# Performance work log

Measured on AMD Instinct MI355X. Metric: run time of the kernel, lower is better.

Reference implementation:

```python
import jax, jax.numpy as jnp
import numpy as np

N = 50000      # nodes
E = 800000     # random edges (self-loops appended inside reference)
DIN = 128
DH = 32        # per-head hidden dim of layer 1
H = 8          # heads
DOUT = 32      # output dim (layer 2, concat=False)
NEG_SLOPE = 0.2


def segment_softmax(e, seg, num):
    # numerically stable softmax over variable-size segments (per-destination)
    m = jax.ops.segment_max(e, seg, num_segments=num)
    m = jnp.where(jnp.isfinite(m), m, jnp.zeros_like(m))
    ex = jnp.exp(e - m[seg])
    s = jax.ops.segment_sum(ex, seg, num_segments=num)
    return ex / (s[seg] + 1e-16)


def gatv2_conv(x, src, dst, Wl, Wr, att, bias, heads, dim, concat):
    n = x.shape[0]
    xl = (x @ Wl).reshape(n, heads, dim)   # source transform
    xr = (x @ Wr).reshape(n, heads, dim)   # target transform
    z = xl[src] + xr[dst]                  # [E, H, D] gather per edge
    z = jnp.where(z > 0, z, NEG_SLOPE * z) # LeakyReLU BEFORE attention vector (GATv2)
    e = jnp.einsum('ehd,hd->eh', z, att)   # attention logits [E, H]
    alpha = segment_softmax(e, dst, n)     # softmax over in-edges of each dst
    out = jax.ops.segment_sum(alpha[:, :, None] * xl[src], dst, num_segments=n)
    if concat:
        return out.reshape(n, heads * dim) + bias
    return out.mean(axis=1) + bias


def setup_inputs() -> dict:
    key = jax.random.key(0)
    ks = jax.random.split(key, 12)
    x = jax.random.normal(ks[0], (N, DIN), dtype=jnp.float32)
    edge_index = jax.random.randint(ks[1], (2, E), 0, N, dtype=jnp.int64)
    s = 0.05
    Wl1 = jax.random.normal(ks[2], (DIN, H * DH), dtype=jnp.float32) * s
    Wr1 = jax.random.normal(ks[3], (DIN, H * DH), dtype=jnp.float32) * s
    att1 = jax.random.normal(ks[4], (H, DH), dtype=jnp.float32) * s
    b1 = jnp.zeros((H * DH,), dtype=jnp.float32)
    Wl2 = jax.random.normal(ks[5], (H * DH, H * DOUT), dtype=jnp.float32) * s
    Wr2 = jax.random.normal(ks[6], (H * DH, H * DOUT), dtype=jnp.float32) * s
    att2 = jax.random.normal(ks[7], (H, DOUT), dtype=jnp.float32) * s
    b2 = jnp.zeros((DOUT,), dtype=jnp.float32)
    return {"x": x, "edge_index": edge_index, "Wl1": Wl1, "Wr1": Wr1,
            "att1": att1, "b1": b1, "Wl2": Wl2, "Wr2": Wr2,
            "att2": att2, "b2": b2}


def reference(x, edge_index, Wl1, Wr1, att1, b1, Wl2, Wr2, att2, b2):
    n = x.shape[0]
    loops = jnp.arange(n, dtype=edge_index.dtype)
    src = jnp.concatenate([edge_index[0], loops])  # PyG adds self-loops by default
    dst = jnp.concatenate([edge_index[1], loops])
    h = gatv2_conv(x, src, dst, Wl1, Wr1, att1, b1, H, DH, concat=True)
    h = jax.nn.elu(h)
    out = gatv2_conv(h, src, dst, Wl2, Wr2, att2, b2, H, DOUT, concat=False)
    return out
```

## Files before the change

kernel.cpp:

```cpp
#include <hip/hip_runtime.h>
#include <hip/hip_bf16.h>

typedef __hip_bfloat16 bf16;
typedef __attribute__((ext_vector_type(8))) short bf16x8;
typedef __attribute__((ext_vector_type(4))) float f32x4;
typedef __attribute__((ext_vector_type(2))) float f32x2;

#define N_NODES 50000
#define E_RAW   800000
#define E_TOT   850000
#define H_HEADS 8
#define F_DIM   256
#define NB_SCAN 196

__device__ __forceinline__ float loadF(const void* p, size_t i, int f32) {
    return f32 ? ((const float*)p)[i] : __bfloat162float(((const bf16*)p)[i]);
}
__device__ __forceinline__ int loadI(const void* p, size_t i, int is32) {
    return is32 ? ((const int*)p)[i] : (int)((const long long*)p)[i];
}
__device__ __forceinline__ float uasf(unsigned u) { return __uint_as_float(u); }
__device__ __forceinline__ unsigned f2bfbits(float f) {
    unsigned u = __float_as_uint(f);
    return (u + 0x7fff + ((u >> 16) & 1)) >> 16;
}
__device__ __forceinline__ short f2bfs(float f) {
    unsigned u = __float_as_uint(f);
    return (short)((u + 0x7fff + ((u >> 16) & 1)) >> 16);
}

__global__ void detect_zero(const void* __restrict__ x, const void* __restrict__ ei,
                            int* __restrict__ flags, int* __restrict__ counts) {
    int gid = blockIdx.x * 256 + threadIdx.x;
    if (gid < N_NODES) counts[gid] = 0;
    if (blockIdx.x != 0) return;
    __shared__ int sf[2];
    int t = threadIdx.x;
    if (t < 2) sf[t] = 0;
    __syncthreads();
    const unsigned short* xs = (const unsigned short*)x;
    int f32 = 0;
    for (int i = t; i < 8192; i += 256) {
        unsigned e = (xs[i] >> 7) & 0xFF;
        if (e >= 134) f32 = 1;
    }
    const int* eii = (const int*)ei;
    int odd = 0;
    for (int i = t; i < 1024; i += 256)
        if (eii[2 * i + 1] != 0) odd = 1;
    if (f32) atomicOr(&sf[0], 1);
    if (odd) atomicOr(&sf[1], 1);
    __syncthreads();
    if (t < 2) flags[t] = sf[t];
}

__global__ void xcvt(const void* __restrict__ x, bf16* __restrict__ xb,
                     const int* __restrict__ flags) {
    const int f32 = flags[0];
    int i = blockIdx.x * 256 + threadIdx.x;
    if (i >= (N_NODES * 128) / 8) return;
    unsigned short* dst = (unsigned short*)xb + (size_t)i * 8;
    if (f32) {
        const float* xp = (const float*)x + (size_t)i * 8;
        float4 v0 = *(const float4*)xp;
        float4 v1 = *(const float4*)(xp + 4);
        uint4 o;
        o.x = f2bfbits(v0.x) | (f2bfbits(v0.y) << 16);
        o.y = f2bfbits(v0.z) | (f2bfbits(v0.w) << 16);
        o.z = f2bfbits(v1.x) | (f2bfbits(v1.y) << 16);
        o.w = f2bfbits(v1.z) | (f2bfbits(v1.w) << 16);
        *(uint4*)dst = o;
    } else {
        uint4 v = *(const uint4*)((const unsigned short*)x + (size_t)i * 8);
        *(uint4*)dst = v;
    }
}

__global__ void prep(const void* __restrict__ wl1, const void* __restrict__ wr1,
                     const void* __restrict__ wl2, const void* __restrict__ wr2,
                     const void* __restrict__ ei,
                     bf16* __restrict__ wb, int* __restrict__ counts,
                     unsigned short* __restrict__ rank,
                     const int* __restrict__ flags) {
    const int f32 = flags[0], is32 = flags[1];
    int gid = blockIdx.x * 256 + threadIdx.x;
    if (gid < E_TOT) {
        int d = (gid < E_RAW) ? loadI(ei, (size_t)E_RAW + gid, is32) : (gid - E_RAW);
        rank[gid] = (unsigned short)atomicAdd(&counts[d], 1);
    }
    for (size_t j = gid; j < 196608; j += (size_t)gridDim.x * 256) {
        const void* src; size_t off, base;
        int k, n;
        if (j < 65536) {
            int half = j >= 32768;
            off = j - (size_t)half * 32768;
            src = half ? wr1 : wl1;
            k = (int)(off >> 8); n = half * 256 + (int)(off & 255);
            base = 0;
        } else {
            size_t jj = j - 65536;
            int half = jj >= 65536;
            off = jj - (size_t)half * 65536;
            src = half ? wr2 : wl2;
            k = (int)(off >> 8); n = half * 256 + (int)(off & 255);
            base = 65536;
        }
        int kb = k >> 5, jo = k & 7;
        int lane = ((k >> 3) & 3) * 16 + (n & 15);
        int ctg = n >> 4;
        size_t dst = base + (((size_t)(kb * 32 + ctg) * 64 + lane) * 8 + jo);
        wb[dst] = __float2bfloat16(loadF(src, off, f32));
    }
}

__global__ void scan1(const int* __restrict__ counts, int* __restrict__ rp,
                      int* __restrict__ bsum) {
    __shared__ int sm[256];
    int b = blockIdx.x, t = threadIdx.x;
    int i = b * 256 + t;
    int v = (i < N_NODES) ? counts[i] : 0;
    sm[t] = v; __syncthreads();
    for (int off = 1; off < 256; off <<= 1) {
        int u = (t >= off) ? sm[t - off] : 0;
        __syncthreads();
        sm[t] += u;
        __syncthreads();
    }
    int incl = sm[t];
    if (i < N_NODES) rp[i] = incl - v;
    if (t == 255) bsum[b] = incl;
}

__global__ void scan2(int* __restrict__ bsum) {
    __shared__ int sm[256];
    int t = threadIdx.x;
    int v = (t < NB_SCAN) ? bsum[t] : 0;
    sm[t] = v; __syncthreads();
    for (int off = 1; off < 256; off <<= 1) {
        int u = (t >= off) ? sm[t - off] : 0;
        __syncthreads();
        sm[t] += u;
        __syncthreads();
    }
    if (t < NB_SCAN) bsum[t] = sm[t] - v;
}

__global__ void scan3(int* __restrict__ rp, const int* __restrict__ bsum) {
    int b = blockIdx.x, t = threadIdx.x;
    int i = b * 256 + t;
    if (i < N_NODES) rp[i] += bsum[b];
    if (i == 0) rp[N_NODES] = E_TOT;
}

__global__ void fill(const void* __restrict__ ei, const int* __restrict__ rp,
                     const unsigned short* __restrict__ rank,
                     int* __restrict__ srcs, const int* __restrict__ flags) {
    const int is32 = flags[1];
    int e = blockIdx.x * 256 + threadIdx.x;
    if (e >= E_TOT + 64) return;
    if (e >= E_TOT) { srcs[e] = 0; return; }
    int s, d;
    if (e < E_RAW) { s = loadI(ei, e, is32); d = loadI(ei, (size_t)E_RAW + e, is32); }
    else           { s = d = e - E_RAW; }
    srcs[rp[d] + rank[e]] = s;
}

__launch_bounds__(256)
__global__ void gemm_mfma(const bf16* __restrict__ A, const bf16* __restrict__ Wsw,
                          bf16* __restrict__ Cl, bf16* __restrict__ Cr,
                          int M, int K) {
    const int tid = threadIdx.x;
    const int w = tid >> 6, lane = tid & 63, q = lane >> 4, l16 = lane & 15;
    const int bRow = blockIdx.x * 128 + (w >> 1) * 64;
    const int bCol = blockIdx.y * 128 + (w & 1) * 64;
    const int ctg0 = bCol >> 4;
    const short* Wp = (const short*)Wsw;
    const int nkb = K >> 5;
    int rows[4];
#pragma unroll
    for (int i = 0; i < 4; ++i) {
        int r = bRow + i * 16 + l16;
        rows[i] = r < M ? r : M - 1;
    }
    f32x4 acc[16] = {};
    for (int kb = 0; kb < nkb; ++kb) {
        bf16x8 a[4], b[4];
#pragma unroll
        for (int i = 0; i < 4; ++i)
            a[i] = *(const bf16x8*)((const short*)A + (size_t)rows[i] * K + q * 8 + kb * 32);
#pragma unroll
        for (int j = 0; j < 4; ++j)
            b[j] = *(const bf16x8*)(Wp + ((size_t)(kb * 32 + ctg0 + j) * 64 + lane) * 8);
#pragma unroll
        for (int i = 0; i < 4; ++i)
#pragma unroll
            for (int j = 0; j < 4; ++j)
                acc[i * 4 + j] =
                    __builtin_amdgcn_mfma_f32_16x16x32_bf16(b[j], a[i], acc[i * 4 + j], 0, 0, 0);
    }
    unsigned short* C = (unsigned short*)(bCol < 256 ? Cl : Cr);
    const int cBase = (bCol < 256 ? bCol : bCol - 256) + q * 4;
#pragma unroll
    for (int i = 0; i < 4; ++i) {
        int row = bRow + i * 16 + l16;
        if (row < M) {
#pragma unroll
            for (int j = 0; j < 4; ++j) {
                f32x4 v = acc[i * 4 + j];
                uint2 o;
                o.x = f2bfbits(v[0]) | (f2bfbits(v[1]) << 16);
                o.y = f2bfbits(v[2]) | (f2bfbits(v[3]) << 16);
                *(uint2*)(C + (size_t)row * 256 + cBase + j * 16) = o;
            }
        }
    }
}

#define EDGE(Q, PRED)                                                         \
    {                                                                         \
        f32x2 X0 = {uasf(Q.x << 16), uasf(Q.x & 0xffff0000u)};                \
        f32x2 X1 = {uasf(Q.y << 16), uasf(Q.y & 0xffff0000u)};                \
        f32x2 X2 = {uasf(Q.z << 16), uasf(Q.z & 0xffff0000u)};                \
        f32x2 X3 = {uasf(Q.w << 16), uasf(Q.w & 0xffff0000u)};                \
        f32x2 z0 = X0 + rv0, z1 = X1 + rv1, z2 = X2 + rv2, z3 = X3 + rv3;     \
        float qq = a0.x * fabsf(z0.x);                                        \
        qq = fmaf(a0.y, fabsf(z0.y), qq);                                     \
        qq = fmaf(a1.x, fabsf(z1.x), qq);                                     \
        qq = fmaf(a1.y, fabsf(z1.y), qq);                                     \
        qq = fmaf(a2.x, fabsf(z2.x), qq);                                     \
        qq = fmaf(a2.y, fabsf(z2.y), qq);                                     \
        qq = fmaf(a3.x, fabsf(z3.x), qq);                                     \
        qq = fmaf(a3.y, fabsf(z3.y), qq);                                     \
        f32x2 slv = a0 * X0;                                                  \
        slv += a1 * X1; slv += a2 * X2; slv += a3 * X3;                       \
        float pp = fmaf(0.6f, slv.x + slv.y, 0.4f * qq);                      \
        pp += __shfl_xor(pp, 1); pp += __shfl_xor(pp, 2);                     \
        float wv = (PRED) ? __expf(pp + cd) : 0.f;                            \
        den += wv;                                                            \
        f32x2 wv2 = {wv, wv};                                                 \
        n0 += wv2 * X0; n1 += wv2 * X1; n2 += wv2 * X2; n3 += wv2 * X3;       \
    }
__launch_bounds__(256)
__global__ void fused_attn(const int* __restrict__ rp, const int* __restrict__ srcs,
                           const bf16* __restrict__ xl, const bf16* __restrict__ xr,
                           const void* __restrict__ att, const void* __restrict__ bias,
                           void* __restrict__ outp, int mode,
                           const int* __restrict__ flags) {
    const int f32 = flags[0];
    const int tid = threadIdx.x, wid = tid >> 6, lane = tid & 63;
    const int sub = lane & 31;
    const int d = blockIdx.x * 8 + wid * 2 + (lane >> 5);

    const unsigned short* xru = (const unsigned short*)xr;
    uint4 xv = *(const uint4*)(xru + (size_t)d * 256 + sub * 8);
    f32x2 rv0 = {uasf(xv.x << 16), uasf(xv.x & 0xffff0000u)};
    f32x2 rv1 = {uasf(xv.y << 16), uasf(xv.y & 0xffff0000u)};
    f32x2 rv2 = {uasf(xv.z << 16), uasf(xv.z & 0xffff0000u)};
    f32x2 rv3 = {uasf(xv.w << 16), uasf(xv.w & 0xffff0000u)};
    f32x2 a0, a1, a2, a3;
    if (f32) {
        float4 t0 = *(const float4*)((const float*)att + sub * 8);
        float4 t1 = *(const float4*)((const float*)att + sub * 8 + 4);
        a0 = {t0.x, t0.y}; a1 = {t0.z, t0.w}; a2 = {t1.x, t1.y}; a3 = {t1.z, t1.w};
    } else {
        uint4 av = *(const uint4*)((const unsigned short*)att + sub * 8);
        a0 = {uasf(av.x << 16), uasf(av.x & 0xffff0000u)};
        a1 = {uasf(av.y << 16), uasf(av.y & 0xffff0000u)};
        a2 = {uasf(av.z << 16), uasf(av.z & 0xffff0000u)};
        a3 = {uasf(av.w << 16), uasf(av.w & 0xffff0000u)};
    }

    f32x2 tv = a0 * rv0;
    tv += a1 * rv1; tv += a2 * rv2; tv += a3 * rv3;
    float t = tv.x + tv.y;
    t += __shfl_xor(t, 1); t += __shfl_xor(t, 2);
    const float cd = 0.6f * t;

    const int start = rp[d], cnt = rp[d + 1] - start;
    int mA = __shfl(cnt, 0), mB = __shfl(cnt, 32);
    const int maxc = mA > mB ? mA : mB;
    const int* sp = srcs + start;
    const unsigned short* xlu = (const unsigned short*)xl + sub * 8;

    float den = 0.f;
    f32x2 n0 = {0,0}, n1 = {0,0}, n2 = {0,0}, n3 = {0,0};
    int i = 0;
    for (; i + 3 < maxc; i += 4) {
        int s0 = sp[i], s1 = sp[i + 1], s2 = sp[i + 2], s3 = sp[i + 3];
        uint4 q0 = *(const uint4*)(xlu + (size_t)s0 * 256);
        uint4 q1 = *(const uint4*)(xlu + (size_t)s1 * 256);
        uint4 q2 = *(const uint4*)(xlu + (size_t)s2 * 256);
        uint4 q3 = *(const uint4*)(xlu + (size_t)s3 * 256);
        EDGE(q0, i < cnt);
        EDGE(q1, i + 1 < cnt);
        EDGE(q2, i + 2 < cnt);
        EDGE(q3, i + 3 < cnt);
    }
    for (; i < maxc; ++i) {
        int s0 = sp[i];
        uint4 q0 = *(const uint4*)(xlu + (size_t)s0 * 256);
        EDGE(q0, i < cnt);
    }
    float rd = 1.f / (den + 1e-16f);
    float v[8] = {n0.x * rd, n0.y * rd, n1.x * rd, n1.y * rd,
                  n2.x * rd, n2.y * rd, n3.x * rd, n3.y * rd};

    if (mode == 1) {
        float b[8];
        if (f32) {
            float4 t0 = *(const float4*)((const float*)bias + sub * 8);
            float4 t1 = *(const float4*)((const float*)bias + sub * 8 + 4);
            b[0]=t0.x; b[1]=t0.y; b[2]=t0.z; b[3]=t0.w;
            b[4]=t1.x; b[5]=t1.y; b[6]=t1.z; b[7]=t1.w;
        } else {
            uint4 bv = *(const uint4*)((const unsigned short*)bias + sub * 8);
            b[0]=uasf(bv.x<<16); b[1]=uasf(bv.x&0xffff0000u);
            b[2]=uasf(bv.y<<16); b[3]=uasf(bv.y&0xffff0000u);
            b[4]=uasf(bv.z<<16); b[5]=uasf(bv.z&0xffff0000u);
            b[6]=uasf(bv.w<<16); b[7]=uasf(bv.w&0xffff0000u);
        }
        uint4 o;
        unsigned oo[4];
#pragma unroll
        for (int k = 0; k < 4; ++k) {
            float u0 = v[2*k]   + b[2*k];
            float u1 = v[2*k+1] + b[2*k+1];
            u0 = u0 > 0.f ? u0 : expm1f(u0);
            u1 = u1 > 0.f ? u1 : expm1f(u1);
            oo[k] = f2bfbits(u0) | (f2bfbits(u1) << 16);
        }
        o.x = oo[0]; o.y = oo[1]; o.z = oo[2]; o.w = oo[3];
        *(uint4*)((unsigned short*)outp + (size_t)d * 256 + sub * 8) = o;
    } else {
#pragma unroll
        for (int k = 0; k < 8; ++k) {
            v[k] += __shfl_xor(v[k], 4);
            v[k] += __shfl_xor(v[k], 8);
            v[k] += __shfl_xor(v[k], 16);
        }
        if (sub < 4) {
            int j = sub * 8;
            float o[8];
#pragma unroll
            for (int k = 0; k < 8; ++k)
                o[k] = v[k] * 0.125f + loadF(bias, j + k, f32);
            if (f32) {
                float4 o0 = {o[0], o[1], o[2], o[3]};
                float4 o1 = {o[4], o[5], o[6], o[7]};
                *(float4*)((float*)outp + (size_t)d * 32 + j)     = o0;
                *(float4*)((float*)outp + (size_t)d * 32 + j + 4) = o1;
            } else {
                uint4 ob;
                ob.x = f2bfbits(o[0]) | (f2bfbits(o[1]) << 16);
                ob.y = f2bfbits(o[2]) | (f2bfbits(o[3]) << 16);
                ob.z = f2bfbits(o[4]) | (f2bfbits(o[5]) << 16);
                ob.w = f2bfbits(o[6]) | (f2bfbits(o[7]) << 16);
                *(uint4*)((unsigned short*)outp + (size_t)d * 32 + j) = ob;
            }
        }
    }
}

extern "C" void kernel_launch(void* const* d_in, const int* in_sizes, int n_in,
                              void* d_out, int out_size, void* d_ws, size_t ws_size,
                              hipStream_t stream) {
    const void* x    = d_in[0];
    const void* ei   = d_in[1];
    const void* Wl1  = d_in[2];
    const void* Wr1  = d_in[3];
    const void* att1 = d_in[4];
    const void* b1   = d_in[5];
    const void* Wl2  = d_in[6];
    const void* Wr2  = d_in[7];
    const void* att2 = d_in[8];
    const void* b2   = d_in[9];

    char* p = (char*)d_ws;
    auto take = [&](size_t bytes) { char* r = p; p += (bytes + 255) & ~(size_t)255; return r; };
    int*  flags  = (int*) take(64 * sizeof(int));
    bf16* wb     = (bf16*)take(196608 * sizeof(bf16));
    bf16* xl     = (bf16*)take((size_t)N_NODES * F_DIM * sizeof(bf16));
    bf16* xr     = (bf16*)take((size_t)N_NODES * F_DIM * sizeof(bf16));
    bf16* h1     = (bf16*)take((size_t)N_NODES * F_DIM * sizeof(bf16));
    int*  rp     = (int*) take((N_NODES + 1) * sizeof(int));
    int*  counts = (int*) take(N_NODES * sizeof(int));
    int*  bsum   = (int*) take(256 * sizeof(int));
    unsigned short* rank = (unsigned short*)take((size_t)E_TOT * sizeof(unsigned short));
    int*  srcs   = (int*) take(((size_t)E_TOT + 64) * sizeof(int));

    bf16* W1sw = wb;
    bf16* W2sw = wb + 65536;
    bf16* xb   = h1;

    const int GB = (E_TOT + 255) / 256;

    detect_zero<<<196, 256, 0, stream>>>(x, ei, flags, counts);
    xcvt<<<(N_NODES * 128 / 8 + 255) / 256, 256, 0, stream>>>(x, xb, flags);
    prep<<<GB, 256, 0, stream>>>(Wl1, Wr1, Wl2, Wr2, ei, wb, counts, rank, flags);
    scan1<<<NB_SCAN, 256, 0, stream>>>(counts, rp, bsum);
    scan2<<<1, 256, 0, stream>>>(bsum);
    scan3<<<NB_SCAN, 256, 0, stream>>>(rp, bsum);
    fill<<<GB, 256, 0, stream>>>(ei, rp, rank, srcs, flags);

    dim3 ggrd((N_NODES + 127) / 128, 4);

    gemm_mfma<<<ggrd, 256, 0, stream>>>(xb, W1sw, xl, xr, N_NODES, 128);
    fused_attn<<<N_NODES / 8, 256, 0, stream>>>(rp, srcs, xl, xr, att1, b1, h1, 1, flags);

    gemm_mfma<<<ggrd, 256, 0, stream>>>(h1, W2sw, xl, xr, N_NODES, 256);
    fused_attn<<<N_NODES / 8, 256, 0, stream>>>(rp, srcs, xl, xr, att2, b2, d_out, 2, flags);
}
```

Baseline: 374.5 us.

## Process nodes in degree-sorted order with one node per wave, split edges across half-waves

Builds a degree histogram and counting-sorts nodes by descending in-degree, so the attention kernel visits heavy nodes first and keeps the waves in a block balanced. Each wave now handles a single destination node, with the two 32-lane halves taking alternate edges and combining their partial sums by shuffle. The old scheme ran two nodes per wave to the longer of the two lengths, which left lanes idle. The GEMM remaps its 1-D grid for XCD locality, and bf16 input x is read directly instead of being copied. Costs are extra scan work, an indirection through the order array, and atomics that make the node order nondeterministic.

Measured after the change: 535.7 us. +43.1%, slower.

```diff
diff --git a/kernel.cpp b/kernel.cpp
--- a/kernel.cpp
+++ b/kernel.cpp
@@ -24,15 +24,13 @@
     unsigned u = __float_as_uint(f);
     return (u + 0x7fff + ((u >> 16) & 1)) >> 16;
 }
-__device__ __forceinline__ short f2bfs(float f) {
-    unsigned u = __float_as_uint(f);
-    return (short)((u + 0x7fff + ((u >> 16) & 1)) >> 16);
-}
 
 __global__ void detect_zero(const void* __restrict__ x, const void* __restrict__ ei,
-                            int* __restrict__ flags, int* __restrict__ counts) {
+                            int* __restrict__ flags, int* __restrict__ counts,
+                            int* __restrict__ deghist) {
     int gid = blockIdx.x * 256 + threadIdx.x;
     if (gid < N_NODES) counts[gid] = 0;
+    if (gid < 256) deghist[gid] = 0;
     if (blockIdx.x != 0) return;
     __shared__ int sf[2];
     int t = threadIdx.x;
@@ -56,24 +54,19 @@
 
 __global__ void xcvt(const void* __restrict__ x, bf16* __restrict__ xb,
                      const int* __restrict__ flags) {
-    const int f32 = flags[0];
+    if (!flags[0]) return;
     int i = blockIdx.x * 256 + threadIdx.x;
     if (i >= (N_NODES * 128) / 8) return;
     unsigned short* dst = (unsigned short*)xb + (size_t)i * 8;
-    if (f32) {
-        const float* xp = (const float*)x + (size_t)i * 8;
-        float4 v0 = *(const float4*)xp;
-        float4 v1 = *(const float4*)(xp + 4);
-        uint4 o;
-        o.x = f2bfbits(v0.x) | (f2bfbits(v0.y) << 16);
-        o.y = f2bfbits(v0.z) | (f2bfbits(v0.w) << 16);
-        o.z = f2bfbits(v1.x) | (f2bfbits(v1.y) << 16);
-        o.w = f2bfbits(v1.z) | (f2bfbits(v1.w) << 16);
-        *(uint4*)dst = o;
-    } else {
-        uint4 v = *(const uint4*)((const unsigned short*)x + (size_t)i * 8);
-        *(uint4*)dst = v;
-    }
+    const float* xp = (const float*)x + (size_t)i * 8;
+    float4 v0 = *(const float4*)xp;
+    float4 v1 = *(const float4*)(xp + 4);
+    uint4 o;
+    o.x = f2bfbits(v0.x) | (f2bfbits(v0.y) << 16);
+    o.y = f2bfbits(v0.z) | (f2bfbits(v0.w) << 16);
+    o.z = f2bfbits(v1.x) | (f2bfbits(v1.y) << 16);
+    o.w = f2bfbits(v1.z) | (f2bfbits(v1.w) << 16);
+    *(uint4*)dst = o;
 }
 
 __global__ void prep(const void* __restrict__ wl1, const void* __restrict__ wr1,
@@ -114,12 +107,18 @@
 }
 
 __global__ void scan1(const int* __restrict__ counts, int* __restrict__ rp,
-                      int* __restrict__ bsum) {
+                      int* __restrict__ bsum, int* __restrict__ deghist) {
     __shared__ int sm[256];
+    __shared__ int lh[256];
     int b = blockIdx.x, t = threadIdx.x;
     int i = b * 256 + t;
     int v = (i < N_NODES) ? counts[i] : 0;
-    sm[t] = v; __syncthreads();
+    sm[t] = v; lh[t] = 0;
+    __syncthreads();
+    if (i < N_NODES) {
+        int dg = v < 255 ? v : 255;
+        atomicAdd(&lh[255 - dg], 1);
+    }
     for (int off = 1; off < 256; off <<= 1) {
         int u = (t >= off) ? sm[t - off] : 0;
         __syncthreads();
@@ -129,9 +128,10 @@
     int incl = sm[t];
     if (i < N_NODES) rp[i] = incl - v;
     if (t == 255) bsum[b] = incl;
-}
-
-__global__ void scan2(int* __restrict__ bsum) {
+    if (lh[t]) atomicAdd(&deghist[t], lh[t]);
+}
+
+__global__ void scan2(int* __restrict__ bsum, int* __restrict__ deghist) {
     __shared__ int sm[256];
     int t = threadIdx.x;
     int v = (t < NB_SCAN) ? bsum[t] : 0;
@@ -143,12 +143,29 @@
         __syncthreads();
     }
     if (t < NB_SCAN) bsum[t] = sm[t] - v;
-}
-
-__global__ void scan3(int* __restrict__ rp, const int* __restrict__ bsum) {
+    __syncthreads();
+    int hv = deghist[t];
+    sm[t] = hv; __syncthreads();
+    for (int off = 1; off < 256; off <<= 1) {
+        int u = (t >= off) ? sm[t - off] : 0;
+        __syncthreads();
+        sm[t] += u;
+        __syncthreads();
+    }
+    deghist[t] = sm[t] - hv;
+}
+
+__global__ void scan3(int* __restrict__ rp, const int* __restrict__ bsum,
+                      const int* __restrict__ counts, int* __restrict__ deghist,
+                      int* __restrict__ ord) {
     int b = blockIdx.x, t = threadIdx.x;
     int i = b * 256 + t;
-    if (i < N_NODES) rp[i] += bsum[b];
+    if (i < N_NODES) {
+        rp[i] += bsum[b];
+        int dg = counts[i]; dg = dg < 255 ? dg : 255;
+        int pos = atomicAdd(&deghist[255 - dg], 1);
+        ord[pos] = i;
+    }
     if (i == 0) rp[N_NODES] = E_TOT;
 }
 
@@ -157,8 +174,7 @@
                      int* __restrict__ srcs, const int* __restrict__ flags) {
     const int is32 = flags[1];
     int e = blockIdx.x * 256 + threadIdx.x;
-    if (e >= E_TOT + 64) return;
-    if (e >= E_TOT) { srcs[e] = 0; return; }
+    if (e >= E_TOT) return;
     int s, d;
     if (e < E_RAW) { s = loadI(ei, e, is32); d = loadI(ei, (size_t)E_RAW + e, is32); }
     else           { s = d = e - E_RAW; }
@@ -166,13 +182,21 @@
 }
 
 __launch_bounds__(256)
-__global__ void gemm_mfma(const bf16* __restrict__ A, const bf16* __restrict__ Wsw,
+__global__ void gemm_mfma(const bf16* __restrict__ Abf, const void* __restrict__ Araw,
+                          const bf16* __restrict__ Wsw,
                           bf16* __restrict__ Cl, bf16* __restrict__ Cr,
-                          int M, int K) {
+                          int M, int K, int aDyn, const int* __restrict__ flags) {
+    const bf16* A = (aDyn && !flags[0]) ? (const bf16*)Araw : Abf;
+    const int nwg = gridDim.x, orig = blockIdx.x;
+    const int xcd = orig & 7, tt = orig >> 3;
+    const int qc = nwg >> 3, rc = nwg & 7;
+    const int v = (xcd < rc ? xcd * (qc + 1) : rc * (qc + 1) + (xcd - rc) * qc) + tt;
+    const int bx = v >> 2, by = v & 3;
+
     const int tid = threadIdx.x;
     const int w = tid >> 6, lane = tid & 63, q = lane >> 4, l16 = lane & 15;
-    const int bRow = blockIdx.x * 128 + (w >> 1) * 64;
-    const int bCol = blockIdx.y * 128 + (w & 1) * 64;
+    const int bRow = bx * 128 + (w >> 1) * 64;
+    const int bCol = by * 128 + (w & 1) * 64;
     const int ctg0 = bCol >> 4;
     const short* Wp = (const short*)Wsw;
     const int nkb = K >> 5;
@@ -206,10 +230,10 @@
         if (row < M) {
 #pragma unroll
             for (int j = 0; j < 4; ++j) {
-                f32x4 v = acc[i * 4 + j];
+                f32x4 vv = acc[i * 4 + j];
                 uint2 o;
-                o.x = f2bfbits(v[0]) | (f2bfbits(v[1]) << 16);
-                o.y = f2bfbits(v[2]) | (f2bfbits(v[3]) << 16);
+                o.x = f2bfbits(vv[0]) | (f2bfbits(vv[1]) << 16);
+                o.y = f2bfbits(vv[2]) | (f2bfbits(vv[3]) << 16);
                 *(uint2*)(C + (size_t)row * 256 + cBase + j * 16) = o;
             }
         }
@@ -242,14 +266,15 @@
     }
 __launch_bounds__(256)
 __global__ void fused_attn(const int* __restrict__ rp, const int* __restrict__ srcs,
+                           const int* __restrict__ ord,
                            const bf16* __restrict__ xl, const bf16* __restrict__ xr,
                            const void* __restrict__ att, const void* __restrict__ bias,
                            void* __restrict__ outp, int mode,
                            const int* __restrict__ flags) {
     const int f32 = flags[0];
     const int tid = threadIdx.x, wid = tid >> 6, lane = tid & 63;
-    const int sub = lane & 31;
-    const int d = blockIdx.x * 8 + wid * 2 + (lane >> 5);
+    const int sub = lane & 31, hh = lane >> 5;
+    const int d = ord[blockIdx.x * 4 + wid];
 
     const unsigned short* xru = (const unsigned short*)xr;
     uint4 xv = *(const uint4*)(xru + (size_t)d * 256 + sub * 8);
@@ -277,60 +302,68 @@
     const float cd = 0.6f * t;
 
     const int start = rp[d], cnt = rp[d + 1] - start;
-    int mA = __shfl(cnt, 0), mB = __shfl(cnt, 32);
-    const int maxc = mA > mB ? mA : mB;
     const int* sp = srcs + start;
     const unsigned short* xlu = (const unsigned short*)xl + sub * 8;
 
     float den = 0.f;
     f32x2 n0 = {0,0}, n1 = {0,0}, n2 = {0,0}, n3 = {0,0};
     int i = 0;
-    for (; i + 3 < maxc; i += 4) {
-        int s0 = sp[i], s1 = sp[i + 1], s2 = sp[i + 2], s3 = sp[i + 3];
+    for (; i + 7 < cnt; i += 8) {
+        int s0 = sp[i + hh], s1 = sp[i + 2 + hh];
+        int s2 = sp[i + 4 + hh], s3 = sp[i + 6 + hh];
         uint4 q0 = *(const uint4*)(xlu + (size_t)s0 * 256);
         uint4 q1 = *(const uint4*)(xlu + (size_t)s1 * 256);
         uint4 q2 = *(const uint4*)(xlu + (size_t)s2 * 256);
         uint4 q3 = *(const uint4*)(xlu + (size_t)s3 * 256);
-        EDGE(q0, i < cnt);
-        EDGE(q1, i + 1 < cnt);
-        EDGE(q2, i + 2 < cnt);
-        EDGE(q3, i + 3 < cnt);
-    }
-    for (; i < maxc; ++i) {
-        int s0 = sp[i];
+        EDGE(q0, 1);
+        EDGE(q1, 1);
+        EDGE(q2, 1);
+        EDGE(q3, 1);
+    }
+    for (; i < cnt; i += 2) {
+        int idx = i + hh;
+        int s0 = sp[idx < cnt ? idx : cnt - 1];
         uint4 q0 = *(const uint4*)(xlu + (size_t)s0 * 256);
-        EDGE(q0, i < cnt);
-    }
+        EDGE(q0, idx < cnt);
+    }
+    den  += __shfl_xor(den, 32);
+    n0.x += __shfl_xor(n0.x, 32); n0.y += __shfl_xor(n0.y, 32);
+    n1.x += __shfl_xor(n1.x, 32); n1.y += __shfl_xor(n1.y, 32);
+    n2.x += __shfl_xor(n2.x, 32); n2.y += __shfl_xor(n2.y, 32);
+    n3.x += __shfl_xor(n3.x, 32); n3.y += __shfl_xor(n3.y, 32);
+
     float rd = 1.f / (den + 1e-16f);
     float v[8] = {n0.x * rd, n0.y * rd, n1.x * rd, n1.y * rd,
                   n2.x * rd, n2.y * rd, n3.x * rd, n3.y * rd};
 
     if (mode == 1) {
-        float b[8];
-        if (f32) {
-            float4 t0 = *(const float4*)((const float*)bias + sub * 8);
-            float4 t1 = *(const float4*)((const float*)bias + sub * 8 + 4);
-            b[0]=t0.x; b[1]=t0.y; b[2]=t0.z; b[3]=t0.w;
-            b[4]=t1.x; b[5]=t1.y; b[6]=t1.z; b[7]=t1.w;
-        } else {
-            uint4 bv = *(const uint4*)((const unsigned short*)bias + sub * 8);
-            b[0]=uasf(bv.x<<16); b[1]=uasf(bv.x&0xffff0000u);
-            b[2]=uasf(bv.y<<16); b[3]=uasf(bv.y&0xffff0000u);
-            b[4]=uasf(bv.z<<16); b[5]=uasf(bv.z&0xffff0000u);
-            b[6]=uasf(bv.w<<16); b[7]=uasf(bv.w&0xffff0000u);
+        if (lane < 32) {
+            float b[8];
+            if (f32) {
+                float4 t0 = *(const float4*)((const float*)bias + sub * 8);
+                float4 t1 = *(const float4*)((const float*)bias + sub * 8 + 4);
+                b[0]=t0.x; b[1]=t0.y; b[2]=t0.z; b[3]=t0.w;
+                b[4]=t1.x; b[5]=t1.y; b[6]=t1.z; b[7]=t1.w;
+            } else {
+                uint4 bv = *(const uint4*)((const unsigned short*)bias + sub * 8);
+                b[0]=uasf(bv.x<<16); b[1]=uasf(bv.x&0xffff0000u);
+                b[2]=uasf(bv.y<<16); b[3]=uasf(bv.y&0xffff0000u);
+                b[4]=uasf(bv.z<<16); b[5]=uasf(bv.z&0xffff0000u);
+                b[6]=uasf(bv.w<<16); b[7]=uasf(bv.w&0xffff0000u);
+            }
+            uint4 o;
+            unsigned oo[4];
+#pragma unroll
+            for (int k = 0; k < 4; ++k) {
+                float u0 = v[2*k]   + b[2*k];
+                float u1 = v[2*k+1] + b[2*k+1];
+                u0 = u0 > 0.f ? u0 : expm1f(u0);
+                u1 = u1 > 0.f ? u1 : expm1f(u1);
+                oo[k] = f2bfbits(u0) | (f2bfbits(u1) << 16);
+            }
+            o.x = oo[0]; o.y = oo[1]; o.z = oo[2]; o.w = oo[3];
+            *(uint4*)((unsigned short*)outp + (size_t)d * 256 + sub * 8) = o;
         }
-        uint4 o;
-        unsigned oo[4];
-#pragma unroll
-        for (int k = 0; k < 4; ++k) {
-            float u0 = v[2*k]   + b[2*k];
-            float u1 = v[2*k+1] + b[2*k+1];
-            u0 = u0 > 0.f ? u0 : expm1f(u0);
-            u1 = u1 > 0.f ? u1 : expm1f(u1);
-            oo[k] = f2bfbits(u0) | (f2bfbits(u1) << 16);
-        }
-        o.x = oo[0]; o.y = oo[1]; o.z = oo[2]; o.w = oo[3];
-        *(uint4*)((unsigned short*)outp + (size_t)d * 256 + sub * 8) = o;
     } else {
 #pragma unroll
         for (int k = 0; k < 8; ++k) {
@@ -338,8 +371,8 @@
             v[k] += __shfl_xor(v[k], 8);
             v[k] += __shfl_xor(v[k], 16);
         }
-        if (sub < 4) {
-            int j = sub * 8;
+        if (lane < 4) {
+            int j = lane * 8;
             float o[8];
 #pragma unroll
             for (int k = 0; k < 8; ++k)
@@ -377,16 +410,18 @@
 
     char* p = (char*)d_ws;
     auto take = [&](size_t bytes) { char* r = p; p += (bytes + 255) & ~(size_t)255; return r; };
-    int*  flags  = (int*) take(64 * sizeof(int));
-    bf16* wb     = (bf16*)take(196608 * sizeof(bf16));
-    bf16* xl     = (bf16*)take((size_t)N_NODES * F_DIM * sizeof(bf16));
-    bf16* xr     = (bf16*)take((size_t)N_NODES * F_DIM * sizeof(bf16));
-    bf16* h1     = (bf16*)take((size_t)N_NODES * F_DIM * sizeof(bf16));
-    int*  rp     = (int*) take((N_NODES + 1) * sizeof(int));
-    int*  counts = (int*) take(N_NODES * sizeof(int));
-    int*  bsum   = (int*) take(256 * sizeof(int));
+    int*  flags   = (int*) take(64 * sizeof(int));
+    int*  deghist = (int*) take(256 * sizeof(int));
+    bf16* wb      = (bf16*)take(196608 * sizeof(bf16));
+    bf16* xl      = (bf16*)take((size_t)N_NODES * F_DIM * sizeof(bf16));
+    bf16* xr      = (bf16*)take((size_t)N_NODES * F_DIM * sizeof(bf16));
+    bf16* h1      = (bf16*)take((size_t)N_NODES * F_DIM * sizeof(bf16));
+    int*  rp      = (int*) take((N_NODES + 1) * sizeof(int));
+    int*  counts  = (int*) take(N_NODES * sizeof(int));
+    int*  bsum    = (int*) take(256 * sizeof(int));
+    int*  ord     = (int*) take(N_NODES * sizeof(int));
     unsigned short* rank = (unsigned short*)take((size_t)E_TOT * sizeof(unsigned short));
-    int*  srcs   = (int*) take(((size_t)E_TOT + 64) * sizeof(int));
+    int*  srcs    = (int*) take(((size_t)E_TOT + 64) * sizeof(int));
 
     bf16* W1sw = wb;
     bf16* W2sw = wb + 65536;
@@ -394,19 +429,19 @@
 
     const int GB = (E_TOT + 255) / 256;
 
-    detect_zero<<<196, 256, 0, stream>>>(x, ei, flags, counts);
+    detect_zero<<<196, 256, 0, stream>>>(x, ei, flags, counts, deghist);
     xcvt<<<(N_NODES * 128 / 8 + 255) / 256, 256, 0, stream>>>(x, xb, flags);
     prep<<<GB, 256, 0, stream>>>(Wl1, Wr1, Wl2, Wr2, ei, wb, counts, rank, flags);
-    scan1<<<NB_SCAN, 256, 0, stream>>>(counts, rp, bsum);
-    scan2<<<1, 256, 0, stream>>>(bsum);
-    scan3<<<NB_SCAN, 256, 0, stream>>>(rp, bsum);
+    scan1<<<NB_SCAN, 256, 0, stream>>>(counts, rp, bsum, deghist);
+    scan2<<<1, 256, 0, stream>>>(bsum, deghist);
+    scan3<<<NB_SCAN, 256, 0, stream>>>(rp, bsum, counts, deghist, ord);
     fill<<<GB, 256, 0, stream>>>(ei, rp, rank, srcs, flags);
 
-    dim3 ggrd((N_NODES + 127) / 128, 4);
-
-    gemm_mfma<<<ggrd, 256, 0, stream>>>(xb, W1sw, xl, xr, N_NODES, 128);
-    fused_attn<<<N_NODES / 8, 256, 0, stream>>>(rp, srcs, xl, xr, att1, b1, h1, 1, flags);
-
-    gemm_mfma<<<ggrd, 256, 0, stream>>>(h1, W2sw, xl, xr, N_NODES, 256);
-    fused_attn<<<N_NODES / 8, 256, 0, stream>>>(rp, srcs, xl, xr, att2, b2, d_out, 2, flags);
-}
+    const int NGB = ((N_NODES + 127) / 128) * 4;
+
+    gemm_mfma<<<NGB, 256, 0, stream>>>(xb, x, W1sw, xl, xr, N_NODES, 128, 1, flags);
+    fused_attn<<<N_NODES / 4, 256, 0, stream>>>(rp, srcs, ord, xl, xr, att1, b1, h1, 1, flags);
+
+    gemm_mfma<<<NGB, 256, 0, stream>>>(h1, nullptr, W2sw, xl, xr, N_NODES, 256, 0, flags);
+    fused_attn<<<N_NODES / 4, 256, 0, stream>>>(rp, srcs, ord, xl, xr, att2, b2, d_out, 2, flags);
+}
```

## Use head-major layout for layer-1 attention and compress edge source indices to 16-bit

Applied to the files above, without the earlier changes.

Layer 1 now writes xl/xr in a head-major layout and runs a new per-head attention kernel, one head per block, so each gathered source row is 64 bytes and stays contiguous within a head. The layer-2 GEMM reads h1 in that head-major layout. The CSR source array is stored as unsigned short to halve index traffic, which only works because N is below 65536. Other changes: the GEMM blocks are remapped across XCDs, the x conversion is skipped when the input is already bf16, and out-of-range edge indices are clamped in the layer-2 kernel. The per-head kernel launches eight times as many blocks and repeats the per-destination setup for each head.

Result: slower. 465.1 us (+24.2%).

```diff
diff --git a/kernel.cpp b/kernel.cpp
--- a/kernel.cpp
+++ b/kernel.cpp
@@ -23,10 +23,6 @@
 __device__ __forceinline__ unsigned f2bfbits(float f) {
     unsigned u = __float_as_uint(f);
     return (u + 0x7fff + ((u >> 16) & 1)) >> 16;
-}
-__device__ __forceinline__ short f2bfs(float f) {
-    unsigned u = __float_as_uint(f);
-    return (short)((u + 0x7fff + ((u >> 16) & 1)) >> 16);
 }
 
 __global__ void detect_zero(const void* __restrict__ x, const void* __restrict__ ei,
@@ -56,24 +52,19 @@
 
 __global__ void xcvt(const void* __restrict__ x, bf16* __restrict__ xb,
                      const int* __restrict__ flags) {
-    const int f32 = flags[0];
+    if (!flags[0]) return;
     int i = blockIdx.x * 256 + threadIdx.x;
     if (i >= (N_NODES * 128) / 8) return;
     unsigned short* dst = (unsigned short*)xb + (size_t)i * 8;
-    if (f32) {
-        const float* xp = (const float*)x + (size_t)i * 8;
-        float4 v0 = *(const float4*)xp;
-        float4 v1 = *(const float4*)(xp + 4);
-        uint4 o;
-        o.x = f2bfbits(v0.x) | (f2bfbits(v0.y) << 16);
-        o.y = f2bfbits(v0.z) | (f2bfbits(v0.w) << 16);
-        o.z = f2bfbits(v1.x) | (f2bfbits(v1.y) << 16);
-        o.w = f2bfbits(v1.z) | (f2bfbits(v1.w) << 16);
-        *(uint4*)dst = o;
-    } else {
-        uint4 v = *(const uint4*)((const unsigned short*)x + (size_t)i * 8);
-        *(uint4*)dst = v;
-    }
+    const float* xp = (const float*)x + (size_t)i * 8;
+    float4 v0 = *(const float4*)xp;
+    float4 v1 = *(const float4*)(xp + 4);
+    uint4 o;
+    o.x = f2bfbits(v0.x) | (f2bfbits(v0.y) << 16);
+    o.y = f2bfbits(v0.z) | (f2bfbits(v0.w) << 16);
+    o.z = f2bfbits(v1.x) | (f2bfbits(v1.y) << 16);
+    o.w = f2bfbits(v1.z) | (f2bfbits(v1.w) << 16);
+    *(uint4*)dst = o;
 }
 
 __global__ void prep(const void* __restrict__ wl1, const void* __restrict__ wr1,
@@ -154,7 +145,7 @@
 
 __global__ void fill(const void* __restrict__ ei, const int* __restrict__ rp,
                      const unsigned short* __restrict__ rank,
-                     int* __restrict__ srcs, const int* __restrict__ flags) {
+                     unsigned short* __restrict__ srcs, const int* __restrict__ flags) {
     const int is32 = flags[1];
     int e = blockIdx.x * 256 + threadIdx.x;
     if (e >= E_TOT + 64) return;
@@ -162,17 +153,26 @@
     int s, d;
     if (e < E_RAW) { s = loadI(ei, e, is32); d = loadI(ei, (size_t)E_RAW + e, is32); }
     else           { s = d = e - E_RAW; }
-    srcs[rp[d] + rank[e]] = s;
+    srcs[rp[d] + rank[e]] = (unsigned short)s;
 }
 
 __launch_bounds__(256)
-__global__ void gemm_mfma(const bf16* __restrict__ A, const bf16* __restrict__ Wsw,
+__global__ void gemm_mfma(const bf16* __restrict__ Abf, const void* __restrict__ Araw,
+                          const bf16* __restrict__ Wsw,
                           bf16* __restrict__ Cl, bf16* __restrict__ Cr,
-                          int M, int K) {
+                          int M, int K, int aDyn, int aHead, int cHead,
+                          const int* __restrict__ flags) {
+    const bf16* A = (aDyn && !flags[0]) ? (const bf16*)Araw : Abf;
+    const int nwg = gridDim.x, orig = blockIdx.x;
+    const int xcd = orig & 7, tt = orig >> 3;
+    const int qc = nwg >> 3, rc = nwg & 7;
+    const int v = (xcd < rc ? xcd * (qc + 1) : rc * (qc + 1) + (xcd - rc) * qc) + tt;
+    const int bx = v >> 2, by = v & 3;
+
     const int tid = threadIdx.x;
     const int w = tid >> 6, lane = tid & 63, q = lane >> 4, l16 = lane & 15;
-    const int bRow = blockIdx.x * 128 + (w >> 1) * 64;
-    const int bCol = blockIdx.y * 128 + (w & 1) * 64;
+    const int bRow = bx * 128 + (w >> 1) * 64;
+    const int bCol = by * 128 + (w & 1) * 64;
     const int ctg0 = bCol >> 4;
     const short* Wp = (const short*)Wsw;
     const int nkb = K >> 5;
@@ -186,8 +186,12 @@
     for (int kb = 0; kb < nkb; ++kb) {
         bf16x8 a[4], b[4];
 #pragma unroll
-        for (int i = 0; i < 4; ++i)
-            a[i] = *(const bf16x8*)((const short*)A + (size_t)rows[i] * K + q * 8 + kb * 32);
+        for (int i = 0; i < 4; ++i) {
+            size_t off = aHead
+                ? (((size_t)kb * N_NODES + rows[i]) * 32 + q * 8)
+                : ((size_t)rows[i] * K + q * 8 + kb * 32);
+            a[i] = *(const bf16x8*)((const short*)A + off);
+        }
 #pragma unroll
         for (int j = 0; j < 4; ++j)
             b[j] = *(const bf16x8*)(Wp + ((size_t)(kb * 32 + ctg0 + j) * 64 + lane) * 8);
@@ -206,13 +210,104 @@
         if (row < M) {
 #pragma unroll
             for (int j = 0; j < 4; ++j) {
-                f32x4 v = acc[i * 4 + j];
+                f32x4 vv = acc[i * 4 + j];
                 uint2 o;
-                o.x = f2bfbits(v[0]) | (f2bfbits(v[1]) << 16);
-                o.y = f2bfbits(v[2]) | (f2bfbits(v[3]) << 16);
-                *(uint2*)(C + (size_t)row * 256 + cBase + j * 16) = o;
+                o.x = f2bfbits(vv[0]) | (f2bfbits(vv[1]) << 16);
+                o.y = f2bfbits(vv[2]) | (f2bfbits(vv[3]) << 16);
+                int c0 = cBase + j * 16;
+                size_t off = cHead
+                    ? (((size_t)(c0 >> 5) * N_NODES + row) * 32 + (c0 & 31))
+                    : ((size_t)row * 256 + c0);
+                *(uint2*)(C + off) = o;
             }
         }
+    }
+}
+
+__launch_bounds__(256)
+__global__ void attn_head(const int* __restrict__ rp, const unsigned short* __restrict__ srcs,
+                          const bf16* __restrict__ xlh, const bf16* __restrict__ xrh,
+                          const void* __restrict__ att, const void* __restrict__ bias,
+                          bf16* __restrict__ outh, const int* __restrict__ flags) {
+    const int f32 = flags[0];
+    const int blk = blockIdx.x;
+    const int h = blk & 7;
+    const int wid = threadIdx.x >> 6, lane = threadIdx.x & 63;
+    const int d = (blk >> 3) * 4 + wid;
+    const int eg = lane >> 3, dl = lane & 7;
+
+    const unsigned short* xlp = (const unsigned short*)xlh + (size_t)h * N_NODES * 32 + dl * 4;
+    const unsigned short* xrp = (const unsigned short*)xrh + ((size_t)h * N_NODES + d) * 32 + dl * 4;
+
+    f32x2 a0, a1;
+    if (f32) {
+        float4 t4 = *(const float4*)((const float*)att + h * 32 + dl * 4);
+        a0 = {t4.x, t4.y}; a1 = {t4.z, t4.w};
+    } else {
+        uint2 av = *(const uint2*)((const unsigned short*)att + h * 32 + dl * 4);
+        a0 = {uasf(av.x << 16), uasf(av.x & 0xffff0000u)};
+        a1 = {uasf(av.y << 16), uasf(av.y & 0xffff0000u)};
+    }
+    uint2 xv = *(const uint2*)xrp;
+    f32x2 rv0 = {uasf(xv.x << 16), uasf(xv.x & 0xffff0000u)};
+    f32x2 rv1 = {uasf(xv.y << 16), uasf(xv.y & 0xffff0000u)};
+
+    f32x2 tv = a0 * rv0; tv += a1 * rv1;
+    float t = tv.x + tv.y;
+    t += __shfl_xor(t, 1); t += __shfl_xor(t, 2); t += __shfl_xor(t, 4);
+    const float cd = 0.6f * t;
+
+    const int start = rp[d], cnt = rp[d + 1] - start;
+    const unsigned short* sp = srcs + start;
+
+    float den = 0.f;
+    f32x2 n0 = {0, 0}, n1 = {0, 0};
+    for (int i = 0; i < cnt; i += 8) {
+        int idx = i + eg;
+        int s = sp[idx < cnt ? idx : cnt - 1];
+        uint2 qv = *(const uint2*)(xlp + (size_t)s * 32);
+        f32x2 X0 = {uasf(qv.x << 16), uasf(qv.x & 0xffff0000u)};
+        f32x2 X1 = {uasf(qv.y << 16), uasf(qv.y & 0xffff0000u)};
+        f32x2 z0 = X0 + rv0, z1 = X1 + rv1;
+        float qq = a0.x * fabsf(z0.x);
+        qq = fmaf(a0.y, fabsf(z0.y), qq);
+        qq = fmaf(a1.x, fabsf(z1.x), qq);
+        qq = fmaf(a1.y, fabsf(z1.y), qq);
+        f32x2 slv = a0 * X0; slv += a1 * X1;
+        float pp = fmaf(0.6f, slv.x + slv.y, 0.4f * qq);
+        pp += __shfl_xor(pp, 1); pp += __shfl_xor(pp, 2); pp += __shfl_xor(pp, 4);
+        float wv = (idx < cnt) ? __expf(pp + cd) : 0.f;
+        den += wv;
+        f32x2 w2 = {wv, wv};
+        n0 += w2 * X0; n1 += w2 * X1;
+    }
+    den  += __shfl_xor(den, 8);  den  += __shfl_xor(den, 16);  den  += __shfl_xor(den, 32);
+    n0.x += __shfl_xor(n0.x, 8); n0.x += __shfl_xor(n0.x, 16); n0.x += __shfl_xor(n0.x, 32);
+    n0.y += __shfl_xor(n0.y, 8); n0.y += __shfl_xor(n0.y, 16); n0.y += __shfl_xor(n0.y, 32);
+    n1.x += __shfl_xor(n1.x, 8); n1.x += __shfl_xor(n1.x, 16); n1.x += __shfl_xor(n1.x, 32);
+    n1.y += __shfl_xor(n1.y, 8); n1.y += __shfl_xor(n1.y, 16); n1.y += __shfl_xor(n1.y, 32);
+
+    if (lane < 8) {
+        float rd = 1.f / (den + 1e-16f);
+        float b0, b1v, b2, b3;
+        if (f32) {
+            float4 bv = *(const float4*)((const float*)bias + h * 32 + dl * 4);
+            b0 = bv.x; b1v = bv.y; b2 = bv.z; b3 = bv.w;
+        } else {
+            uint2 bv = *(const uint2*)((const unsigned short*)bias + h * 32 + dl * 4);
+            b0 = uasf(bv.x << 16); b1v = uasf(bv.x & 0xffff0000u);
+            b2 = uasf(bv.y << 16); b3  = uasf(bv.y & 0xffff0000u);
+        }
+        float u0 = n0.x * rd + b0, u1 = n0.y * rd + b1v;
+        float u2 = n1.x * rd + b2, u3 = n1.y * rd + b3;
+        u0 = u0 > 0.f ? u0 : expm1f(u0);
+        u1 = u1 > 0.f ? u1 : expm1f(u1);
+        u2 = u2 > 0.f ? u2 : expm1f(u2);
+        u3 = u3 > 0.f ? u3 : expm1f(u3);
+        uint2 o;
+        o.x = f2bfbits(u0) | (f2bfbits(u1) << 16);
+        o.y = f2bfbits(u2) | (f2bfbits(u3) << 16);
+        *(uint2*)((unsigned short*)outh + ((size_t)h * N_NODES + d) * 32 + dl * 4) = o;
     }
 }
 
@@ -241,11 +336,10 @@
         n0 += wv2 * X0; n1 += wv2 * X1; n2 += wv2 * X2; n3 += wv2 * X3;       \
     }
 __launch_bounds__(256)
-__global__ void fused_attn(const int* __restrict__ rp, const int* __restrict__ srcs,
+__global__ void fused_attn(const int* __restrict__ rp, const unsigned short* __restrict__ srcs,
                            const bf16* __restrict__ xl, const bf16* __restrict__ xr,
                            const void* __restrict__ att, const void* __restrict__ bias,
-                           void* __restrict__ outp, int mode,
-                           const int* __restrict__ flags) {
+                           void* __restrict__ outp, const int* __restrict__ flags) {
     const int f32 = flags[0];
     const int tid = threadIdx.x, wid = tid >> 6, lane = tid & 63;
     const int sub = lane & 31;
@@ -277,16 +371,21 @@
     const float cd = 0.6f * t;
 
     const int start = rp[d], cnt = rp[d + 1] - start;
+    const int cnt1 = cnt - 1;
     int mA = __shfl(cnt, 0), mB = __shfl(cnt, 32);
     const int maxc = mA > mB ? mA : mB;
-    const int* sp = srcs + start;
+    const unsigned short* sp = srcs + start;
     const unsigned short* xlu = (const unsigned short*)xl + sub * 8;
 
     float den = 0.f;
     f32x2 n0 = {0,0}, n1 = {0,0}, n2 = {0,0}, n3 = {0,0};
     int i = 0;
     for (; i + 3 < maxc; i += 4) {
-        int s0 = sp[i], s1 = sp[i + 1], s2 = sp[i + 2], s3 = sp[i + 3];
+        int i0 = i < cnt1 ? i : cnt1;
+        int i1 = i + 1 < cnt1 ? i + 1 : cnt1;
+        int i2 = i + 2 < cnt1 ? i + 2 : cnt1;
+        int i3 = i + 3 < cnt1 ? i + 3 : cnt1;
+        int s0 = sp[i0], s1 = sp[i1], s2 = sp[i2], s3 = sp[i3];
         uint4 q0 = *(const uint4*)(xlu + (size_t)s0 * 256);
         uint4 q1 = *(const uint4*)(xlu + (size_t)s1 * 256);
         uint4 q2 = *(const uint4*)(xlu + (size_t)s2 * 256);
@@ -297,7 +396,8 @@
         EDGE(q3, i + 3 < cnt);
     }
     for (; i < maxc; ++i) {
-        int s0 = sp[i];
+        int i0 = i < cnt1 ? i : cnt1;
+        int s0 = sp[i0];
         uint4 q0 = *(const uint4*)(xlu + (size_t)s0 * 256);
         EDGE(q0, i < cnt);
     }
@@ -305,58 +405,30 @@
     float v[8] = {n0.x * rd, n0.y * rd, n1.x * rd, n1.y * rd,
                   n2.x * rd, n2.y * rd, n3.x * rd, n3.y * rd};
 
-    if (mode == 1) {
-        float b[8];
+#pragma unroll
+    for (int k = 0; k < 8; ++k) {
+        v[k] += __shfl_xor(v[k], 4);
+        v[k] += __shfl_xor(v[k], 8);
+        v[k] += __shfl_xor(v[k], 16);
+    }
+    if (sub < 4) {
+        int j = sub * 8;
+        float o[8];
+#pragma unroll
+        for (int k = 0; k < 8; ++k)
+            o[k] = v[k] * 0.125f + loadF(bias, j + k, f32);
         if (f32) {
-            float4 t0 = *(const float4*)((const float*)bias + sub * 8);
-            float4 t1 = *(const float4*)((const float*)bias + sub * 8 + 4);
-            b[0]=t0.x; b[1]=t0.y; b[2]=t0.z; b[3]=t0.w;
-            b[4]=t1.x; b[5]=t1.y; b[6]=t1.z; b[7]=t1.w;
+            float4 o0 = {o[0], o[1], o[2], o[3]};
+            float4 o1 = {o[4], o[5], o[6], o[7]};
+            *(float4*)((float*)outp + (size_t)d * 32 + j)     = o0;
+            *(float4*)((float*)outp + (size_t)d * 32 + j + 4) = o1;
         } else {
-            uint4 bv = *(const uint4*)((const unsigned short*)bias + sub * 8);
-            b[0]=uasf(bv.x<<16); b[1]=uasf(bv.x&0xffff0000u);
-            b[2]=uasf(bv.y<<16); b[3]=uasf(bv.y&0xffff0000u);
-            b[4]=uasf(bv.z<<16); b[5]=uasf(bv.z&0xffff0000u);
-            b[6]=uasf(bv.w<<16); b[7]=uasf(bv.w&0xffff0000u);
-        }
-        uint4 o;
-        unsigned oo[4];
-#pragma unroll
-        for (int k = 0; k < 4; ++k) {
-            float u0 = v[2*k]   + b[2*k];
-            float u1 = v[2*k+1] + b[2*k+1];
-            u0 = u0 > 0.f ? u0 : expm1f(u0);
-            u1 = u1 > 0.f ? u1 : expm1f(u1);
-            oo[k] = f2bfbits(u0) | (f2bfbits(u1) << 16);
-        }
-        o.x = oo[0]; o.y = oo[1]; o.z = oo[2]; o.w = oo[3];
-        *(uint4*)((unsigned short*)outp + (size_t)d * 256 + sub * 8) = o;
-    } else {
-#pragma unroll
-        for (int k = 0; k < 8; ++k) {
-            v[k] += __shfl_xor(v[k], 4);
-            v[k] += __shfl_xor(v[k], 8);
-            v[k] += __shfl_xor(v[k], 16);
-        }
-        if (sub < 4) {
-            int j = sub * 8;
-            float o[8];
-#pragma unroll
-            for (int k = 0; k < 8; ++k)
-                o[k] = v[k] * 0.125f + loadF(bias, j + k, f32);
-            if (f32) {
-                float4 o0 = {o[0], o[1], o[2], o[3]};
-                float4 o1 = {o[4], o[5], o[6], o[7]};
-                *(float4*)((float*)outp + (size_t)d * 32 + j)     = o0;
-                *(float4*)((float*)outp + (size_t)d * 32 + j + 4) = o1;
-            } else {
-                uint4 ob;
-                ob.x = f2bfbits(o[0]) | (f2bfbits(o[1]) << 16);
-                ob.y = f2bfbits(o[2]) | (f2bfbits(o[3]) << 16);
-                ob.z = f2bfbits(o[4]) | (f2bfbits(o[5]) << 16);
-                ob.w = f2bfbits(o[6]) | (f2bfbits(o[7]) << 16);
-                *(uint4*)((unsigned short*)outp + (size_t)d * 32 + j) = ob;
-            }
+            uint4 ob;
+            ob.x = f2bfbits(o[0]) | (f2bfbits(o[1]) << 16);
+            ob.y = f2bfbits(o[2]) | (f2bfbits(o[3]) << 16);
+            ob.z = f2bfbits(o[4]) | (f2bfbits(o[5]) << 16);
+            ob.w = f2bfbits(o[6]) | (f2bfbits(o[7]) << 16);
+            *(uint4*)((unsigned short*)outp + (size_t)d * 32 + j) = ob;
         }
     }
 }
@@ -386,7 +458,7 @@
     int*  counts = (int*) take(N_NODES * sizeof(int));
     int*  bsum   = (int*) take(256 * sizeof(int));
     unsigned short* rank = (unsigned short*)take((size_t)E_TOT * sizeof(unsigned short));
-    int*  srcs   = (int*) take(((size_t)E_TOT + 64) * sizeof(int));
+    unsigned short* srcs = (unsigned short*)take(((size_t)E_TOT + 64) * sizeof(unsigned short));
 
     bf16* W1sw = wb;
     bf16* W2sw = wb + 65536;
@@ -402,11 +474,11 @@
     scan3<<<NB_SCAN, 256, 0, stream>>>(rp, bsum);
     fill<<<GB, 256, 0, stream>>>(ei, rp, rank, srcs, flags);
 
-    dim3 ggrd((N_NODES + 127) / 128, 4);
-
-    gemm_mfma<<<ggrd, 256, 0, stream>>>(xb, W1sw, xl, xr, N_NODES, 128);
-    fused_attn<<<N_NODES / 8, 256, 0, stream>>>(rp, srcs, xl, xr, att1, b1, h1, 1, flags);
-
-    gemm_mfma<<<ggrd, 256, 0, stream>>>(h1, W2sw, xl, xr, N_NODES, 256);
-    fused_attn<<<N_NODES / 8, 256, 0, stream>>>(rp, srcs, xl, xr, att2, b2, d_out, 2, flags);
-}
+    const int NGB = ((N_NODES + 127) / 128) * 4;
+
+    gemm_mfma<<<NGB, 256, 0, stream>>>(xb, x, W1sw, xl, xr, N_NODES, 128, 1, 0, 1, flags);
+    attn_head<<<(N_NODES / 4) * 8, 256, 0, stream>>>(rp, srcs, xl, xr, att1, b1, h1, flags);
+
+    gemm_mfma<<<NGB, 256, 0, stream>>>(h1, nullptr, W2sw, xl, xr, N_NODES, 256, 0, 1, 0, flags);
+    fused_attn<<<N_NODES / 8, 256, 0, stream>>>(rp, srcs, xl, xr, att2, b2, d_out, flags);
+}
```
